# Optimization experiments

Measured on AMD Instinct MI355X. Metric: run time of the kernel, lower is better.

Reference implementation:

```python
import math
import jax, jax.numpy as jnp
import numpy as np

B, T, DIM = 2, 2048, 2048
HEADS, HEAD_DIM = 16, 128
KV_GROUPS = 4
N_KV = HEADS // KV_GROUPS  # 4
LATENT = 512
SEL_TOPK, SEL_HEADS, SEL_DIM = 64, 1, 64
SOFTCAP = 30.0
EPS = 1e-6


def _alibi_slopes(n):
    def pot(p):
        start = 2.0 ** (-(2.0 ** (-(math.log2(p) - 3))))
        return [start * start ** i for i in range(p)]
    if math.log2(n).is_integer():
        return pot(n)
    cp = 2 ** int(math.floor(math.log2(n)))
    s = pot(cp)
    s += _alibi_slopes(2 * cp)[0::2][: n - cp]
    return s


def _alibi_bias(h, t):
    slopes = jnp.asarray(_alibi_slopes(h), jnp.float32)
    pos = jnp.arange(t)
    dist = jnp.clip(pos[:, None] - pos[None, :], 0, None).astype(jnp.float32)  # causal clamp_min(0)
    return -slopes[:, None, None] * dist  # (H,T,T)


def _rope_emb(t, d):
    inv = 1.0 / (10000.0 ** (jnp.arange(0, d, 2, dtype=jnp.float32) / d))
    f = jnp.arange(t, dtype=jnp.float32)[:, None] * inv[None, :]
    return jnp.concatenate([f, f], axis=-1)  # (T, D)


def _apply_rotary(x, emb):
    # x: (B,T,H,D); replicates RotaryPositionalEncoding.apply_rotary exactly
    cos = jnp.cos(emb)[None, :, None, :]
    sin = jnp.sin(emb)[None, :, None, :]
    x1, x2 = x[..., 0::2], x[..., 1::2]
    c, s = cos[..., 0::2], sin[..., 0::2]
    r = jnp.stack([x1 * c - x2 * s, x1 * s + x2 * c], axis=-1)
    return r.reshape(x.shape)


def _rmsnorm(x, w):
    return x * jax.lax.rsqrt(jnp.mean(x * x, axis=-1, keepdims=True) + EPS) * w


def _forward(x, w_q, b_q, w_down, b_down, w_up, b_up, w_o, b_o, qn_w, kn_w, gate_w, gate_b):
    b, t, _ = x.shape
    # MLA projections
    q = (x @ w_q + b_q).reshape(b, t, HEADS, HEAD_DIM)
    kv = (x @ w_down + b_down) @ w_up + b_up  # (B,T,2*N_KV*D)
    k = kv[..., : N_KV * HEAD_DIM].reshape(b, t, N_KV, HEAD_DIM)
    v = kv[..., N_KV * HEAD_DIM:].reshape(b, t, N_KV, HEAD_DIM)
    # QK RMS-norm + RoPE
    q = _rmsnorm(q, qn_w)
    k = _rmsnorm(k, kn_w)
    emb = _rope_emb(t, HEAD_DIM)
    q = _apply_rotary(q, emb)
    k = _apply_rotary(k, emb)
    # GQA expand kv heads
    k = jnp.repeat(k, KV_GROUPS, axis=2)
    v = jnp.repeat(v, KV_GROUPS, axis=2)
    q = q.transpose(0, 2, 1, 3)  # (B,H,T,D)
    k = k.transpose(0, 2, 1, 3)
    v = v.transpose(0, 2, 1, 3)
    # selector top-k mask (detached)
    qs = jax.lax.stop_gradient(q[:, :SEL_HEADS, :, :SEL_DIM].astype(jnp.float32))
    ks = jax.lax.stop_gradient(k[:, :SEL_HEADS, :, :SEL_DIM].astype(jnp.float32))
    s = jnp.einsum('bhqd,bhkd->bhqk', qs, ks) / math.sqrt(SEL_DIM)
    tri = jnp.triu(jnp.ones((t, t), bool), 1)  # future positions
    s = jnp.where(tri, -jnp.inf, s)
    idx = jax.lax.top_k(s, SEL_TOPK)[1]  # (B,hs,T,K)
    sel = jnp.zeros((b, SEL_HEADS, t, t), bool)
    bi = jnp.arange(b)[:, None, None, None]
    hi = jnp.arange(SEL_HEADS)[None, :, None, None]
    ti = jnp.arange(t)[None, None, :, None]
    sel = sel.at[bi, hi, ti, idx].set(True)
    sel = sel | jnp.eye(t, dtype=bool)[None, None]  # always keep diagonal
    sel = sel & ~tri  # causal
    sel = jnp.any(sel, axis=1, keepdims=True)  # broadcast over heads (h_sel < h)
    amask = jnp.where(sel, 0.0, -jnp.inf).astype(jnp.float32)
    # attention with softcap + ALiBi
    scores = jnp.einsum('bhqd,bhkd->bhqk', q, k) / math.sqrt(HEAD_DIM)
    scores = jnp.tanh(scores / SOFTCAP) * SOFTCAP
    scores = scores + _alibi_bias(HEADS, t)[None] + amask
    attn = jax.nn.softmax(scores, axis=-1)
    y = jnp.einsum('bhqk,bhkd->bhqd', attn, v)
    # per-head dense sigmoid gating on output
    gate = jax.nn.sigmoid(jnp.einsum('bhtd,hde->bhte', y, gate_w) + gate_b[None, :, None, :])
    y = (y * gate).transpose(0, 2, 1, 3).reshape(b, t, HEADS * HEAD_DIM)
    return y @ w_o + b_o


def setup_inputs() -> dict:
    key = jax.random.key(0)
    ks = jax.random.split(key, 6)
    sd = 0.02
    return {
        'x': jax.random.normal(ks[0], (B, T, DIM), jnp.float32),
        'w_q': jax.random.normal(ks[1], (DIM, HEADS * HEAD_DIM), jnp.float32) * sd,
        'b_q': jnp.zeros((HEADS * HEAD_DIM,), jnp.float32),
        'w_down': jax.random.normal(ks[2], (DIM, LATENT), jnp.float32) * sd,
        'b_down': jnp.zeros((LATENT,), jnp.float32),
        'w_up': jax.random.normal(ks[3], (LATENT, 2 * N_KV * HEAD_DIM), jnp.float32) * sd,
        'b_up': jnp.zeros((2 * N_KV * HEAD_DIM,), jnp.float32),
        'w_o': jax.random.normal(ks[4], (HEADS * HEAD_DIM, DIM), jnp.float32) * sd,
        'b_o': jnp.zeros((DIM,), jnp.float32),
        'qn_w': jnp.ones((HEAD_DIM,), jnp.float32),
        'kn_w': jnp.ones((HEAD_DIM,), jnp.float32),
        'gate_w': jax.random.normal(ks[5], (HEADS, HEAD_DIM, HEAD_DIM), jnp.float32) * (1.0 / math.sqrt(HEAD_DIM)),
        'gate_b': jnp.zeros((HEADS, HEAD_DIM), jnp.float32),
    }


def reference(x, w_q, b_q, w_down, b_down, w_up, b_up, w_o, b_o, qn_w, kn_w, gate_w, gate_b):
    return _forward(x, w_q, b_q, w_down, b_down, w_up, b_up, w_o, b_o, qn_w, kn_w, gate_w, gate_b)
```

## Files before the change

### kernel.cpp

```cpp
#include <hip/hip_runtime.h>
#include <math.h>

#define T_SEQ 2048
#define BATCH 2
#define NHEADS 16
#define HD 128
#define NKV 4

typedef __bf16 bf16x8 __attribute__((ext_vector_type(8)));
typedef float f32x4 __attribute__((ext_vector_type(4)));

__device__ inline unsigned short bf16rne(float f) {
  unsigned u = __float_as_uint(f);
  unsigned r = (u + 0x7FFFu + ((u >> 16) & 1u)) >> 16;
  return (unsigned short)r;
}

__device__ inline float bflo(unsigned u) {
  return __uint_as_float(u << 16);
}
__device__ inline float bfhi(unsigned u) {
  return __uint_as_float(u & 0xFFFF0000u);
}

__device__ inline void gload_lds16(const void* g, void* l) {
  __builtin_amdgcn_global_load_lds(
      (__attribute__((address_space(1))) void*)const_cast<void*>(g),
      (__attribute__((address_space(3))) void*)l, 16, 0, 0);
}

#define ENC_NEGINF 0x007FFFFFu
__device__ inline unsigned enc32(float v) {
  unsigned u = __float_as_uint(v);
  return (u & 0x80000000u) ? ~u : (u | 0x80000000u);
}

__global__ void rope_table_kernel(float* __restrict__ tab) {
  int t = blockIdx.x;
  int i = threadIdx.x;
  int j = (2 * i) & 63;
  float y = (float)pow(10000.0, (double)j / 64.0);
  float invf = 1.0f / y;
  float angle = (float)t * invf;
  double a = (double)angle;
  tab[(t * 64 + i) * 2 + 0] = (float)cos(a);
  tab[(t * 64 + i) * 2 + 1] = (float)sin(a);
}

__global__ __launch_bounds__(128) void norm_rope_kernel(
    float* __restrict__ base, const float* __restrict__ w,
    const float* __restrict__ tab, int Hloc, int rowStride) {
  int blk = blockIdx.x;
  int h = blk % Hloc;
  int bt = blk / Hloc;
  int t = bt & (T_SEQ - 1);
  float* row = base + (size_t)bt * rowStride + h * HD;
  int d = threadIdx.x;
  float v = row[d];
  __shared__ float red[128];
  red[d] = v * v;
  __syncthreads();
#pragma unroll
  for (int off = 64; off > 0; off >>= 1) {
    if (d < off) red[d] += red[d + off];
    __syncthreads();
  }
  float ssum = red[0];
  __syncthreads();
  float inv = 1.0f / sqrtf(ssum / 128.0f + 1e-6f);
  float xn = v * inv * w[d];
  red[d] = xn;
  __syncthreads();
  int p = d >> 1;
  float c  = tab[(t * 64 + p) * 2 + 0];
  float sn = tab[(t * 64 + p) * 2 + 1];
  float x1 = red[p * 2], x2 = red[p * 2 + 1];
  row[d] = ((d & 1) == 0) ? (x1 * c - x2 * sn) : (x1 * sn + x2 * c);
}

__global__ __launch_bounds__(128) void kvnorm_rope_kernel(
    float* __restrict__ base, const float* __restrict__ w,
    const float* __restrict__ tab, unsigned short* __restrict__ kvb) {
  int blk = blockIdx.x;
  int h = blk % 4;
  int bt = blk / 4;
  int t = bt & (T_SEQ - 1);
  float* row = base + (size_t)bt * 1024 + h * HD;
  int d = threadIdx.x;
  float v = row[d];
  __shared__ float red[128];
  red[d] = v * v;
  __syncthreads();
#pragma unroll
  for (int off = 64; off > 0; off >>= 1) {
    if (d < off) red[d] += red[d + off];
    __syncthreads();
  }
  float ssum = red[0];
  __syncthreads();
  float inv = 1.0f / sqrtf(ssum / 128.0f + 1e-6f);
  float xn = v * inv * w[d];
  red[d] = xn;
  __syncthreads();
  int p = d >> 1;
  float c  = tab[(t * 64 + p) * 2 + 0];
  float sn = tab[(t * 64 + p) * 2 + 1];
  float x1 = red[p * 2], x2 = red[p * 2 + 1];
  float out = ((d & 1) == 0) ? (x1 * c - x2 * sn) : (x1 * sn + x2 * c);
  row[d] = out;
  size_t kb = (size_t)bt * 1024 + h * HD + d;
  kvb[kb] = bf16rne(out);
  float vv = base[(size_t)bt * 1024 + 512 + h * HD + d];
  kvb[(size_t)bt * 1024 + 512 + h * HD + d] = bf16rne(vv);
}

__global__ __launch_bounds__(256) void qnorm_rope_kernel(
    float* __restrict__ base, const float* __restrict__ w,
    const float* __restrict__ tab) {
  int row = blockIdx.x * 4 + (threadIdx.x >> 6);
  int lane = threadIdx.x & 63;
  int h = row & 15;
  int bt = row >> 4;
  int t = bt & (T_SEQ - 1);
  float* rp = base + (size_t)bt * 2048 + h * HD;
  float2 v = *(const float2*)(rp + 2 * lane);
  float ss = v.x * v.x + v.y * v.y;
#pragma unroll
  for (int off = 32; off > 0; off >>= 1) ss += __shfl_xor(ss, off);
  float inv = 1.0f / sqrtf(ss / 128.0f + 1e-6f);
  float2 wv = *(const float2*)(w + 2 * lane);
  float x1 = v.x * inv * wv.x;
  float x2 = v.y * inv * wv.y;
  float2 cs = *(const float2*)(tab + (t * 64 + lane) * 2);
  float2 o;
  o.x = x1 * cs.x - x2 * cs.y;
  o.y = x1 * cs.y + x2 * cs.x;
  *(float2*)(rp + 2 * lane) = o;
}

__global__ __launch_bounds__(256) void sgemm4_kernel(
    const float* __restrict__ A,
    const float* __restrict__ W1, const float* __restrict__ bias1,
    float* __restrict__ C1, int ldw1, int ldc1, int nx1,
    const float* __restrict__ W2, const float* __restrict__ bias2,
    float* __restrict__ C2, int ldw2, int ldc2, int K) {
  __shared__ float As[32][68];
  __shared__ float Bs[32][68];
  int bx = blockIdx.x;
  const float* W; const float* bias; float* C; int ldw, ldc, n0;
  if (bx < nx1) {
    W = W1; bias = bias1; C = C1; ldw = ldw1; ldc = ldc1; n0 = bx * 64;
  } else {
    W = W2; bias = bias2; C = C2; ldw = ldw2; ldc = ldc2;
    n0 = (bx - nx1) * 64;
  }
  int tid = threadIdx.x;
  int tx = tid & 15;
  int ty = tid >> 4;
  int m0 = blockIdx.y * 64;
  int ar = tid >> 2, ac = (tid & 3) * 8;
  int brr = tid >> 3, bc = (tid & 7) * 8;
  const float* Ap = A + (size_t)(m0 + ar) * K + ac;
  const float* Wp = W + (size_t)brr * ldw + n0 + bc;
  float acc[4][4] = {};
  float4 av0 = *(const float4*)(Ap);
  float4 av1 = *(const float4*)(Ap + 4);
  float4 wv0 = *(const float4*)(Wp);
  float4 wv1 = *(const float4*)(Wp + 4);
  for (int k0 = 0; k0 < K; k0 += 32) {
    As[ac + 0][ar] = av0.x; As[ac + 1][ar] = av0.y;
    As[ac + 2][ar] = av0.z; As[ac + 3][ar] = av0.w;
    As[ac + 4][ar] = av1.x; As[ac + 5][ar] = av1.y;
    As[ac + 6][ar] = av1.z; As[ac + 7][ar] = av1.w;
    *(float4*)&Bs[brr][bc] = wv0;
    *(float4*)&Bs[brr][bc + 4] = wv1;
    __syncthreads();
    if (k0 + 32 < K) {
      av0 = *(const float4*)(Ap + k0 + 32);
      av1 = *(const float4*)(Ap + k0 + 36);
      wv0 = *(const float4*)(Wp + (size_t)(k0 + 32) * ldw);
      wv1 = *(const float4*)(Wp + (size_t)(k0 + 32) * ldw + 4);
    }
#pragma unroll
    for (int kk = 0; kk < 32; kk++) {
      float4 a = *(const float4*)&As[kk][ty * 4];
      float4 b = *(const float4*)&Bs[kk][tx * 4];
      float aa[4] = {a.x, a.y, a.z, a.w};
      float bb[4] = {b.x, b.y, b.z, b.w};
#pragma unroll
      for (int i = 0; i < 4; i++)
#pragma unroll
        for (int j = 0; j < 4; j++) acc[i][j] += aa[i] * bb[j];
    }
    __syncthreads();
  }
  float4 bv = *(const float4*)&bias[n0 + tx * 4];
  float bb[4] = {bv.x, bv.y, bv.z, bv.w};
#pragma unroll
  for (int i = 0; i < 4; i++) {
    float4 o;
    o.x = acc[i][0] + bb[0];
    o.y = acc[i][1] + bb[1];
    o.z = acc[i][2] + bb[2];
    o.w = acc[i][3] + bb[3];
    *(float4*)&C[(size_t)(m0 + ty * 4 + i) * ldc + n0 + tx * 4] = o;
  }
}

__global__ __launch_bounds__(256) void mfma_gemm_bt(
    const unsigned short* __restrict__ A,
    const unsigned short* __restrict__ BT,
    const float* __restrict__ bias,
    float* __restrict__ C,
    int M, int N, int K) {
  __shared__ bf16x8 lA[16][64];
  __shared__ bf16x8 lB[16][64];
  int tid = threadIdx.x;
  int w = tid >> 6, lane = tid & 63;
  int m0 = blockIdx.y * 128, n0 = blockIdx.x * 128;
  int wm = w >> 1, wn = w & 1;
  f32x4 acc[4][4] = {};
  int sr = lane & 15;
  int sk = (lane >> 4) * 8;
  const unsigned short* Abase = A + (size_t)(m0 + sr) * K + sk;
  const unsigned short* Bbase = BT + (size_t)(n0 + sr) * K + sk;

  for (int k0 = 0; k0 < K; k0 += 64) {
    __syncthreads();
#pragma unroll
    for (int c = 0; c < 4; c++) {
      int ch = w * 4 + c;
      int tt = ch >> 1, kk = ch & 1;
      gload_lds16(Abase + (size_t)(tt * 16) * K + k0 + kk * 32, &lA[ch][0]);
      gload_lds16(Bbase + (size_t)(tt * 16) * K + k0 + kk * 32, &lB[ch][0]);
    }
    __syncthreads();
#pragma unroll
    for (int kk = 0; kk < 2; kk++) {
      bf16x8 af[4], bfr[4];
#pragma unroll
      for (int t = 0; t < 4; t++) {
        af[t]  = lA[(wm * 4 + t) * 2 + kk][lane];
        bfr[t] = lB[(wn * 4 + t) * 2 + kk][lane];
      }
#pragma unroll
      for (int i = 0; i < 4; i++)
#pragma unroll
        for (int j = 0; j < 4; j++)
          acc[i][j] = __builtin_amdgcn_mfma_f32_16x16x32_bf16(
              af[i], bfr[j], acc[i][j], 0, 0, 0);
    }
  }
  int col0 = n0 + wn * 64 + (lane & 15);
  int row0 = m0 + wm * 64 + (lane >> 4) * 4;
#pragma unroll
  for (int j = 0; j < 4; j++) {
    float bv = bias[col0 + j * 16];
#pragma unroll
    for (int i = 0; i < 4; i++) {
#pragma unroll
      for (int r = 0; r < 4; r++)
        C[(size_t)(row0 + i * 16 + r) * N + col0 + j * 16] = acc[i][j][r] + bv;
    }
  }
}

__global__ __launch_bounds__(256) void convert_bf16_kernel(
    const float* __restrict__ X, unsigned short* __restrict__ Y, int n4) {
  int i = blockIdx.x * 256 + threadIdx.x;
  if (i >= n4) return;
  float4 v = ((const float4*)X)[i];
  ushort4 o;
  o.x = bf16rne(v.x); o.y = bf16rne(v.y);
  o.z = bf16rne(v.z); o.w = bf16rne(v.w);
  ((ushort4*)Y)[i] = o;
}

__global__ __launch_bounds__(256) void transpose_bf16_kernel(
    const float* __restrict__ W, unsigned short* __restrict__ WT,
    int K, int N) {
  __shared__ unsigned short t[32][33];
  int k0 = blockIdx.y * 32, n0 = blockIdx.x * 32;
  int tid = threadIdx.x;
#pragma unroll
  for (int i = 0; i < 4; i++) {
    int idx = tid + i * 256;
    int r = idx >> 5, c = idx & 31;
    t[c][r] = bf16rne(W[(size_t)(k0 + r) * N + n0 + c]);
  }
  __syncthreads();
#pragma unroll
  for (int i = 0; i < 4; i++) {
    int idx = tid + i * 256;
    int r = idx >> 5, c = idx & 31;
    WT[(size_t)(n0 + r) * K + k0 + c] = t[r][c];
  }
}

__global__ __launch_bounds__(256) void score_kernel(
    const float* __restrict__ qsel,
    const float* __restrict__ kv,
    unsigned* __restrict__ S,
    int b) {
  int tc = blockIdx.x, tr = blockIdx.y;
  if (tc > tr || tr == 0) return;
  __shared__ float qsT[64][68];
  __shared__ float ksT[64][68];
  int tid = threadIdx.x;
  int r0 = tr * 64, c0 = tc * 64;
#pragma unroll
  for (int u = 0; u < 16; u++) {
    int idx = u * 256 + tid;
    int row = idx >> 6, d = idx & 63;
    qsT[d][row] = qsel[((size_t)(b * T_SEQ + r0 + row)) * 128 + d];
  }
#pragma unroll
  for (int u = 0; u < 16; u++) {
    int idx = u * 256 + tid;
    int c = idx >> 6, d = idx & 63;
    ksT[d][c] = kv[((size_t)(b * T_SEQ + c0 + c)) * 1024 + d];
  }
  __syncthreads();
  int tx = tid & 15, ty = tid >> 4;
  float acc[4][4] = {};
  for (int d = 0; d < 64; d++) {
    float4 qv = *(const float4*)&qsT[d][ty * 4];
    float4 kx = *(const float4*)&ksT[d][tx * 4];
    float qq[4] = {qv.x, qv.y, qv.z, qv.w};
    float kk[4] = {kx.x, kx.y, kx.z, kx.w};
#pragma unroll
    for (int i = 0; i < 4; i++)
#pragma unroll
      for (int j = 0; j < 4; j++) acc[i][j] += qq[i] * kk[j];
  }
#pragma unroll
  for (int i = 0; i < 4; i++) {
    int r = r0 + ty * 4 + i;
    uint4 o;
    int c = c0 + tx * 4;
    o.x = (c + 0 <= r) ? enc32(acc[i][0] * 0.125f) : ENC_NEGINF;
    o.y = (c + 1 <= r) ? enc32(acc[i][1] * 0.125f) : ENC_NEGINF;
    o.z = (c + 2 <= r) ? enc32(acc[i][2] * 0.125f) : ENC_NEGINF;
    o.w = (c + 3 <= r) ? enc32(acc[i][3] * 0.125f) : ENC_NEGINF;
    *(uint4*)&S[(size_t)r * 2048 + c] = o;
  }
}

__global__ __launch_bounds__(256) void select_topk_kernel(
    const unsigned* __restrict__ S,
    int* __restrict__ sel_cnt, int* __restrict__ sel_idx, int b) {
  int blk = blockIdx.x;
  int r0 = blk * 4;
  int tid = threadIdx.x;

  if (r0 < 64) {
    for (int j = 0; j < 4; j++) {
      int r = r0 + j;
      int row = b * T_SEQ + r;
      if (tid == 0) sel_cnt[row] = r + 1;
      for (int c = tid; c <= r; c += 256) sel_idx[row * 66 + c] = c;
    }
    return;
  }

  int wv = tid >> 6, lane = tid & 63;
  int rr = r0 + wv;
  int row = b * T_SEQ + rr;
  int imax = rr >> 6;

  unsigned e[32];
  const unsigned* Sp = S + (size_t)rr * 2048 + lane;
#pragma unroll
  for (int i = 0; i < 32; i++) e[i] = (i <= imax) ? Sp[i * 64] : ENC_NEGINF;

  unsigned t = 0;
  for (int bit = 31; bit >= 0; --bit) {
    unsigned cand = t | (1u << bit);
    int cnt = 0;
#pragma unroll
    for (int i = 0; i < 32; i++) cnt += (e[i] >= cand) ? 1 : 0;
#pragma unroll
    for (int off = 1; off < 64; off <<= 1) cnt += __shfl_xor(cnt, off);
    if (cnt >= 64) t = cand;
  }

  unsigned long long below = (lane == 63) ? 0x7FFFFFFFFFFFFFFFull
                                          : ((1ull << lane) - 1ull);
  bool hasdiag = false;
  int base = 0;
#pragma unroll
  for (int i = 0; i < 32; i++) {
    int c = i * 64 + lane;
    bool wn = (e[i] > t);
    unsigned long long m = __ballot(wn);
    if (wn) {
      int slot = base + (int)__popcll(m & below);
      sel_idx[(size_t)row * 66 + slot] = c;
      if (c == rr) hasdiag = true;
    }
    base += (int)__popcll(m);
  }
  int g = base;
  int need = 64 - g;
  int tb = 0;
#pragma unroll
  for (int i = 0; i < 32; i++) {
    int c = i * 64 + lane;
    bool tie = (e[i] == t);
    unsigned long long m = __ballot(tie);
    int rank = tb + (int)__popcll(m & below);
    if (tie && rank < need) {
      sel_idx[(size_t)row * 66 + g + rank] = c;
      if (c == rr) hasdiag = true;
    }
    tb += (int)__popcll(m);
  }
  unsigned long long hd = __ballot(hasdiag);
  if (lane == 0) {
    sel_cnt[row] = hd ? 64 : 65;
    if (!hd) sel_idx[(size_t)row * 66 + 64] = rr;
  }
}

__global__ __launch_bounds__(256) void attn_kernel(
    const float* __restrict__ q,
    const unsigned short* __restrict__ kvb,
    const int* __restrict__ sel_cnt, const int* __restrict__ sel_idx,
    float* __restrict__ yg) {
  int blk = blockIdx.x;
  int g = blk & 3;
  int br = blk >> 2;
  int b = br >> 11;
  int r = br & (T_SEQ - 1);
  int tid = threadIdx.x;
  int lane = tid & 63, wv = tid >> 6;
  int H = g * 4 + wv;

  __shared__ unsigned kls[65 * 64];
  __shared__ float pbuf[4][68];
  __shared__ int idxs[66];

  int cnt = sel_cnt[br];
  if (tid < 66) idxs[tid] = (tid < cnt) ? sel_idx[(size_t)br * 66 + tid] : 0;
  __syncthreads();

  for (int c = tid; c < 65 * 16; c += 256) {
    int row = c >> 4, part = c & 15;
    uint4 kd = make_uint4(0u, 0u, 0u, 0u);
    if (row < cnt) {
      const unsigned short* gp = kvb
          + ((size_t)(b * T_SEQ + idxs[row])) * 1024 + g * HD + part * 8;
      kd = *(const uint4*)gp;
    }
    int slot = part ^ (row & 15);
    *(uint4*)&kls[row * 64 + slot * 4] = kd;
  }
  __syncthreads();

  double sd = 1.0;
  for (int i = 0; i <= H; i++) sd *= 0.70710678118654752440;
  float slope = (float)sd;

  const float* qrow = q + (size_t)br * 2048 + H * HD;

  int kidx = idxs[min(lane, cnt - 1)];
  int swz = lane & 15;
  const unsigned* kr = &kls[lane * 64];
  float acc = 0.f;
#pragma unroll
  for (int dd = 0; dd < 16; dd++) {
    uint4 kb = *(const uint4*)&kr[(dd ^ swz) * 4];
    float4 qa = *(const float4*)(qrow + dd * 8);
    float4 qb = *(const float4*)(qrow + dd * 8 + 4);
    acc += qa.x * bflo(kb.x) + qa.y * bfhi(kb.x);
    acc += qa.z * bflo(kb.y) + qa.w * bfhi(kb.y);
    acc += qb.x * bflo(kb.z) + qb.y * bfhi(kb.z);
    acc += qb.z * bflo(kb.w) + qb.w * bfhi(kb.w);
  }
  float sca = acc / sqrtf(128.0f);
  float tch = tanhf(sca / 30.0f) * 30.0f;
  float s = (lane < cnt) ? (tch - slope * (float)(r - kidx)) : -INFINITY;

  float stail = -INFINITY;
  if (cnt == 65) {
    int i64 = idxs[64];
    unsigned u = kls[64 * 64 + lane];
    float2 qt = *(const float2*)(qrow + 2 * lane);
    float ta = qt.x * bflo(u) + qt.y * bfhi(u);
#pragma unroll
    for (int off = 32; off > 0; off >>= 1) ta += __shfl_xor(ta, off);
    stail = tanhf(ta / sqrtf(128.0f) / 30.0f) * 30.0f
            - slope * (float)(r - i64);
  }

  float m = s;
#pragma unroll
  for (int off = 32; off > 0; off >>= 1) m = fmaxf(m, __shfl_xor(m, off));
  m = fmaxf(m, stail);
  float e = (lane < cnt) ? expf(s - m) : 0.f;
  float sum = e;
#pragma unroll
  for (int off = 32; off > 0; off >>= 1) sum += __shfl_xor(sum, off);
  float et = (cnt == 65) ? expf(stail - m) : 0.f;
  sum += et;
  pbuf[wv][lane] = e / sum;
  if (lane == 0) pbuf[wv][64] = et / sum;
  if (lane >= 1 && lane <= 3) pbuf[wv][64 + lane] = 0.f;

  const unsigned short* vbase = kvb + (size_t)b * T_SEQ * 1024 + 512 + g * HD;
  float y0 = 0.f, y1 = 0.f;
  int jmax = (cnt + 3) >> 2;
  for (int j4 = 0; j4 < jmax; j4++) {
    float4 p4 = *(const float4*)&pbuf[wv][j4 * 4];
    float pp[4] = {p4.x, p4.y, p4.z, p4.w};
#pragma unroll
    for (int t = 0; t < 4; t++) {
      int ij = idxs[min(j4 * 4 + t, cnt - 1)];
      unsigned u = *(const unsigned*)(vbase + (size_t)ij * 1024 + 2 * lane);
      y0 += pp[t] * bflo(u);
      y1 += pp[t] * bfhi(u);
    }
  }
  float2 o;
  o.x = y0;
  o.y = y1;
  *(float2*)(yg + (size_t)br * 2048 + H * HD + 2 * lane) = o;
}

__global__ __launch_bounds__(256) void gate_kernel(
    const float* __restrict__ yg, unsigned short* __restrict__ ygb,
    const float* __restrict__ gw, const float* __restrict__ gb) {
  int blk = blockIdx.x;
  int h = blk & 15;
  int bt0 = (blk >> 4) * 16;
  int tid = threadIdx.x;
  __shared__ float ys[16][128];
  for (int i = tid; i < 16 * 128; i += 256) {
    int rr = i >> 7, d = i & 127;
    ys[rr][d] = yg[(size_t)(bt0 + rr) * 2048 + h * HD + d];
  }
  __syncthreads();
  int e = tid & 127;
  int rblk = tid >> 7;
  const float* gwp = gw + (size_t)h * 16384 + e;
  float acc[8] = {};
  for (int d = 0; d < 128; d++) {
    float wval = gwp[(size_t)d * 128];
#pragma unroll
    for (int k = 0; k < 8; k++) acc[k] += ys[rblk * 8 + k][d] * wval;
  }
  float bb = gb[h * 128 + e];
#pragma unroll
  for (int k = 0; k < 8; k++) {
    int rr = rblk * 8 + k;
    float gate = 1.f / (1.f + expf(-(acc[k] + bb)));
    ygb[(size_t)(bt0 + rr) * 2048 + h * HD + e] = bf16rne(ys[rr][e] * gate);
  }
}

extern "C" void kernel_launch(void* const* d_in, const int* in_sizes, int n_in,
                              void* d_out, int out_size, void* d_ws, size_t ws_size,
                              hipStream_t stream) {
  const float* x      = (const float*)d_in[0];
  const float* w_q    = (const float*)d_in[1];
  const float* b_q    = (const float*)d_in[2];
  const float* w_down = (const float*)d_in[3];
  const float* b_down = (const float*)d_in[4];
  const float* w_up   = (const float*)d_in[5];
  const float* b_up   = (const float*)d_in[6];
  const float* w_o    = (const float*)d_in[7];
  const float* b_o    = (const float*)d_in[8];
  const float* qn_w   = (const float*)d_in[9];
  const float* kn_w   = (const float*)d_in[10];
  const float* gate_w = (const float*)d_in[11];
  const float* gate_b = (const float*)d_in[12];

  float* ws    = (float*)d_ws;
  float* kvbuf = ws;
  float* yg    = ws + 4194304;
  float* dlat  = yg;
  float* tab   = ws + 12582912;
  int*   cnt   = (int*)(ws + 12845056);
  int*   sidx  = cnt + 4096;
  float* qsel  = ws + 13120000;
  unsigned short* xb  = (unsigned short*)(ws + 13906432);
  unsigned short* dlatb = xb;
  unsigned short* ygb = xb;
  unsigned* Sbuf = (unsigned*)xb;
  unsigned short* wT  = xb + 8388608;
  unsigned short* wupT = wT;
  unsigned short* kvb  = wT;

  float* qbuf = (float*)d_out;
  const int BT = BATCH * T_SEQ;

  rope_table_kernel<<<T_SEQ, 64, 0, stream>>>(tab);
  convert_bf16_kernel<<<8192, 256, 0, stream>>>(x, xb, 2097152);
  transpose_bf16_kernel<<<dim3(64, 64), 256, 0, stream>>>(w_q, wT, 2048, 2048);
  mfma_gemm_bt<<<dim3(16, 32), 256, 0, stream>>>(xb, wT, b_q, qbuf,
                                                 BT, 2048, 2048);
  sgemm4_kernel<<<dim3(10, 64), 256, 0, stream>>>(
      x, w_q, b_q, qsel, 2048, 128, 2,
      w_down, b_down, dlat, 512, 512, 2048);
  convert_bf16_kernel<<<2048, 256, 0, stream>>>(dlat, dlatb, 524288);
  transpose_bf16_kernel<<<dim3(32, 16), 256, 0, stream>>>(w_up, wupT,
                                                          512, 1024);
  mfma_gemm_bt<<<dim3(8, 32), 256, 0, stream>>>(dlatb, wupT, b_up, kvbuf,
                                                BT, 1024, 512);
  sgemm4_kernel<<<dim3(2, 64), 256, 0, stream>>>(
      dlat, w_up, b_up, kvbuf, 1024, 1024, 2,
      w_up, b_up, kvbuf, 1024, 1024, 512);
  qnorm_rope_kernel<<<BT * 4, 256, 0, stream>>>(qbuf, qn_w, tab);
  norm_rope_kernel<<<BT, 128, 0, stream>>>(qsel, qn_w, tab, 1, 128);
  kvnorm_rope_kernel<<<BT * 4, 128, 0, stream>>>(kvbuf, kn_w, tab, kvb);
  for (int b = 0; b < BATCH; b++) {
    score_kernel<<<dim3(32, 32), 256, 0, stream>>>(qsel, kvbuf, Sbuf, b);
    select_topk_kernel<<<512, 256, 0, stream>>>(Sbuf, cnt, sidx, b);
  }
  attn_kernel<<<BT * 4, 256, 0, stream>>>(qbuf, kvb, cnt, sidx, yg);
  gate_kernel<<<(BT / 16) * 16, 256, 0, stream>>>(yg, ygb, gate_w, gate_b);
  transpose_bf16_kernel<<<dim3(64, 64), 256, 0, stream>>>(w_o, wT, 2048, 2048);
  mfma_gemm_bt<<<dim3(16, 32), 256, 0, stream>>>(ygb, wT, b_o, (float*)d_out,
                                                 BT, 2048, 2048);
}
```

Before: 747.9 us.

## Load W tile directly into registers in fp32 GEMM, halve K tile

The fp32 selector/down-projection GEMM no longer stages the weight tile in shared memory. Each thread now reads its 16x4 W slice straight from global memory into registers. The K tile drops from 32 to 16 and launch bounds request 4 blocks per SM. This cuts LDS traffic and shared memory use to raise occupancy, but loses the software prefetch of W and the sharing of W loads across rows (ty), which leans on L1/L2 caching instead.

```diff
diff --git a/kernel.cpp b/kernel.cpp
--- a/kernel.cpp
+++ b/kernel.cpp
@@ -138,14 +138,14 @@
   *(float2*)(rp + 2 * lane) = o;
 }
 
-__global__ __launch_bounds__(256) void sgemm4_kernel(
+#define BKG 16
+__global__ __launch_bounds__(256, 4) void sgemm6_kernel(
     const float* __restrict__ A,
     const float* __restrict__ W1, const float* __restrict__ bias1,
     float* __restrict__ C1, int ldw1, int ldc1, int nx1,
     const float* __restrict__ W2, const float* __restrict__ bias2,
     float* __restrict__ C2, int ldw2, int ldc2, int K) {
-  __shared__ float As[32][68];
-  __shared__ float Bs[32][68];
+  __shared__ float As[BKG][68];
   int bx = blockIdx.x;
   const float* W; const float* bias; float* C; int ldw, ldc, n0;
   if (bx < nx1) {
@@ -158,35 +158,27 @@
   int tx = tid & 15;
   int ty = tid >> 4;
   int m0 = blockIdx.y * 64;
-  int ar = tid >> 2, ac = (tid & 3) * 8;
-  int brr = tid >> 3, bc = (tid & 7) * 8;
+  int ar = tid >> 2, ac = (tid & 3) * 4;
   const float* Ap = A + (size_t)(m0 + ar) * K + ac;
-  const float* Wp = W + (size_t)brr * ldw + n0 + bc;
+  const float* Wb = W + n0 + tx * 4;
   float acc[4][4] = {};
-  float4 av0 = *(const float4*)(Ap);
-  float4 av1 = *(const float4*)(Ap + 4);
-  float4 wv0 = *(const float4*)(Wp);
-  float4 wv1 = *(const float4*)(Wp + 4);
-  for (int k0 = 0; k0 < K; k0 += 32) {
-    As[ac + 0][ar] = av0.x; As[ac + 1][ar] = av0.y;
-    As[ac + 2][ar] = av0.z; As[ac + 3][ar] = av0.w;
-    As[ac + 4][ar] = av1.x; As[ac + 5][ar] = av1.y;
-    As[ac + 6][ar] = av1.z; As[ac + 7][ar] = av1.w;
-    *(float4*)&Bs[brr][bc] = wv0;
-    *(float4*)&Bs[brr][bc + 4] = wv1;
+  float4 av = *(const float4*)(Ap);
+  for (int k0 = 0; k0 < K; k0 += BKG) {
+    As[ac + 0][ar] = av.x; As[ac + 1][ar] = av.y;
+    As[ac + 2][ar] = av.z; As[ac + 3][ar] = av.w;
     __syncthreads();
-    if (k0 + 32 < K) {
-      av0 = *(const float4*)(Ap + k0 + 32);
-      av1 = *(const float4*)(Ap + k0 + 36);
-      wv0 = *(const float4*)(Wp + (size_t)(k0 + 32) * ldw);
-      wv1 = *(const float4*)(Wp + (size_t)(k0 + 32) * ldw + 4);
-    }
-#pragma unroll
-    for (int kk = 0; kk < 32; kk++) {
+    float4 breg[BKG];
+#pragma unroll
+    for (int kk = 0; kk < BKG; kk++)
+      breg[kk] = *(const float4*)(Wb + (size_t)(k0 + kk) * ldw);
+    if (k0 + BKG < K) {
+      av = *(const float4*)(Ap + k0 + BKG);
+    }
+#pragma unroll
+    for (int kk = 0; kk < BKG; kk++) {
       float4 a = *(const float4*)&As[kk][ty * 4];
-      float4 b = *(const float4*)&Bs[kk][tx * 4];
       float aa[4] = {a.x, a.y, a.z, a.w};
-      float bb[4] = {b.x, b.y, b.z, b.w};
+      float bb[4] = {breg[kk].x, breg[kk].y, breg[kk].z, breg[kk].w};
 #pragma unroll
       for (int i = 0; i < 4; i++)
 #pragma unroll
@@ -599,7 +591,7 @@
   transpose_bf16_kernel<<<dim3(64, 64), 256, 0, stream>>>(w_q, wT, 2048, 2048);
   mfma_gemm_bt<<<dim3(16, 32), 256, 0, stream>>>(xb, wT, b_q, qbuf,
                                                  BT, 2048, 2048);
-  sgemm4_kernel<<<dim3(10, 64), 256, 0, stream>>>(
+  sgemm6_kernel<<<dim3(10, 64), 256, 0, stream>>>(
       x, w_q, b_q, qsel, 2048, 128, 2,
       w_down, b_down, dlat, 512, 512, 2048);
   convert_bf16_kernel<<<2048, 256, 0, stream>>>(dlat, dlatb, 524288);
@@ -607,7 +599,7 @@
                                                           512, 1024);
   mfma_gemm_bt<<<dim3(8, 32), 256, 0, stream>>>(dlatb, wupT, b_up, kvbuf,
                                                 BT, 1024, 512);
-  sgemm4_kernel<<<dim3(2, 64), 256, 0, stream>>>(
+  sgemm6_kernel<<<dim3(2, 64), 256, 0, stream>>>(
       dlat, w_up, b_up, kvbuf, 1024, 1024, 2,
       w_up, b_up, kvbuf, 1024, 1024, 512);
   qnorm_rope_kernel<<<BT * 4, 256, 0, stream>>>(qbuf, qn_w, tab);
```

After: 824.5 us. +10.2%, slower.
